# Kernel tuning notes

Hardware: AMD Instinct MI355X
Metric: run time of the kernel (lower is better)

Reference implementation:

```python
import jax, jax.numpy as jnp
import numpy as np

EMB_DIM = 128
MID = 192  # ceil(1.5 * emb_dim)
VOCAB = 3000
KCLS = 5
B = 16
S = 128
EPS = 1e-5


def _linear_init(k, fin, fout):
    k1, k2 = jax.random.split(k)
    bound = 1.0 / np.sqrt(fin)
    W = jax.random.uniform(k1, (fin, fout), minval=-bound, maxval=bound, dtype=jnp.float32)
    b = jax.random.uniform(k2, (fout,), minval=-bound, maxval=bound, dtype=jnp.float32)
    return W, b


def setup_inputs() -> dict:
    key = jax.random.key(0)
    ks = jax.random.split(key, 7)
    emb = jax.random.normal(ks[0], (VOCAB, EMB_DIM), dtype=jnp.float32)
    W1, b1 = _linear_init(ks[1], 2 * EMB_DIM, MID)   # encoder layer 1
    W2, b2 = _linear_init(ks[2], MID, EMB_DIM)       # encoder layer 2
    W3, b3 = _linear_init(ks[3], EMB_DIM, MID)       # decoder layer 1
    W4, b4 = _linear_init(ks[4], MID, 2 * EMB_DIM)   # decoder layer 2
    Wk, bk = _linear_init(ks[5], EMB_DIM, KCLS)      # soft head
    inputs = jax.random.randint(ks[6], (B, S), 0, VOCAB, dtype=jnp.int64)
    return dict(inputs=inputs, emb=emb, W1=W1, b1=b1, W2=W2, b2=b2,
                W3=W3, b3=b3, W4=W4, b4=b4, Wk=Wk, bk=bk)


def _forward(inputs, emb, W1, b1, W2, b2, W3, b3, W4, b4, Wk, bk):
    X = emb[inputs]                      # (B,S,m)
    Bs, Sl, m = X.shape
    bidx = jnp.arange(Bs)
    karr = jnp.arange(Sl)
    jarr = jnp.arange(Sl - 1)

    def step(carry, t):
        nodes, counts, acc = carry       # (B,S,m), (B,S), (B,)
        L = Sl - t                       # current active list length
        right, left = nodes[:, 1:], nodes[:, :-1]          # pair j = (node[j+1], node[j])
        y = (jnp.concatenate([right, left], -1) @ W1 + b1) @ W2 + b2   # (B,S-1,m)
        xx = (y @ W3 + b3) @ W4 + b4                                    # (B,S-1,2m)
        # torch cross_entropy with float-vector target: -sum(target * log_softmax(input))
        ls1 = -(right * jax.nn.log_softmax(xx[..., :m], -1)).sum(-1)
        ls2 = -(left * jax.nn.log_softmax(xx[..., m:], -1)).sum(-1)
        n1, n2 = counts[:, 1:], counts[:, :-1]
        loss = ((n1 + EPS) * ls1 + (n2 + EPS) * ls2) / (n1 + n2 + EPS)
        valid = jarr < (L - 1)                                          # only first L-1 pairs active
        idx = jnp.argmin(jnp.where(valid[None, :], loss, jnp.inf), axis=1)  # (B,)
        acc = acc + jnp.take_along_axis(loss, idx[:, None], 1)[:, 0]
        father_x = jnp.take_along_axis(y, idx[:, None, None], 1)[:, 0]  # (B,m)
        # faithful bug: lc = nodelist[idx-1] (python wrap to L-1 when idx==0), rc = nodelist[idx]
        lc_idx = jnp.where(idx == 0, L - 1, idx - 1)
        father_cnt = (jnp.take_along_axis(counts, idx[:, None], 1)[:, 0]
                      + jnp.take_along_axis(counts, lc_idx[:, None], 1)[:, 0])
        pos = jnp.maximum(idx - 1, 0)
        # new list: drop lc and rc, father lands at pos; gather map reproduces list insert/remove
        src = jnp.where((idx[:, None] == 0) | (karr[None, :] < idx[:, None] - 1),
                        karr[None, :], karr[None, :] + 1)
        src = jnp.minimum(src, Sl - 1)
        nodes = jnp.take_along_axis(nodes, src[:, :, None], 1).at[bidx, pos].set(father_x)
        counts = jnp.take_along_axis(counts, src, 1).at[bidx, pos].set(father_cnt)
        return (nodes, counts, acc), None

    init = (X, jnp.ones((Bs, Sl), X.dtype), jnp.zeros((Bs,), X.dtype))
    (nodes, counts, acc), _ = jax.lax.scan(step, init, jnp.arange(Sl - 1))
    pred = jnp.argmax(nodes[:, 0] @ Wk + bk, axis=-1)   # argmax softmax == argmax logits
    return pred, acc.sum() / Bs


def reference(inputs, emb, W1, b1, W2, b2, W3, b3, W4, b4, Wk, bk):
    return _forward(inputs, emb, W1, b1, W2, b2, W3, b3, W4, b4, Wk, bk)
```

## Files before the change

kernel.cpp:

```cpp
#include <hip/hip_runtime.h>
#include <math.h>

#define EMB 128
#define MID 192
#define SEQ 128
#define BATCH 16
#define NPAIR 127
#define KCLS 5
#define EPSF 1e-5f

#define OFF_WYT   0
#define OFF_BY    32768
#define OFF_WXXT  32896
#define OFF_BXX   65664
#define OFF_NODES 65920
#define OFF_YC    328064
#define OFF_L0    588160

__global__ void k_comp(const float* __restrict__ W1, const float* __restrict__ b1,
                       const float* __restrict__ W2, const float* __restrict__ b2,
                       const float* __restrict__ W3, const float* __restrict__ b3,
                       const float* __restrict__ W4, const float* __restrict__ b4,
                       float* __restrict__ ws) {
    int tid = blockIdx.x * blockDim.x + threadIdx.x;
    if (tid < 32768) {
        int k = tid >> 7, o = tid & 127;
        float a = 0.f;
        for (int j = 0; j < MID; ++j) a += W1[k*MID+j] * W2[j*EMB+o];
        int q = k >> 6, jj = k & 63;
        ws[OFF_WYT + (size_t)(q*128 + o)*64 + jj] = a;
    } else if (tid < 65536) {
        int t = tid - 32768;
        int k = t >> 8, c = t & 255;
        float a = 0.f;
        for (int j = 0; j < MID; ++j) a += W3[k*MID+j] * W4[j*256+c];
        int hh = k >> 6, jj = k & 63;
        ws[OFF_WXXT + (size_t)(hh*256 + c)*64 + jj] = a;
    } else if (tid < 65536 + 128) {
        int o = tid - 65536;
        float a = b2[o];
        for (int j = 0; j < MID; ++j) a += b1[j] * W2[j*EMB+o];
        ws[OFF_BY + o] = a;
    } else if (tid < 65536 + 128 + 256) {
        int o = tid - 65536 - 128;
        float a = b4[o];
        for (int j = 0; j < MID; ++j) a += b3[j] * W4[j*256+o];
        ws[OFF_BXX + o] = a;
    }
}

__global__ void k_nodes(const int* __restrict__ inp, const float* __restrict__ emb,
                        float* __restrict__ ws) {
    int tid = blockIdx.x * blockDim.x + threadIdx.x;
    if (tid >= BATCH*SEQ*EMB) return;
    int d = tid & 127;
    int bs = tid >> 7;
    int tok = inp[bs];
    ws[OFF_NODES + tid] = emb[tok*EMB + d];
}

__global__ void __launch_bounds__(512, 2) k_init(float* __restrict__ ws) {
    __shared__ float s_x[2][2*EMB];
    __shared__ float s_red[4][2][EMB];
    __shared__ float s_redx[2][2][256];
    __shared__ float s_y[2][EMB];
    __shared__ float s_by[EMB];
    __shared__ float s_bxx[2*EMB];
    __shared__ float s_ls[2][2];
    int tid = threadIdx.x;
    int b = blockIdx.x >> 3, g = blockIdx.x & 7;
    float wy[64], wxx[64];
    {
        const float4* gw = (const float4*)(ws + OFF_WYT) + (size_t)tid*16;
        #pragma unroll
        for (int i = 0; i < 16; ++i) { float4 v = gw[i]; wy[4*i]=v.x; wy[4*i+1]=v.y; wy[4*i+2]=v.z; wy[4*i+3]=v.w; }
        const float4* gx = (const float4*)(ws + OFF_WXXT) + (size_t)tid*16;
        #pragma unroll
        for (int i = 0; i < 16; ++i) { float4 v = gx[i]; wxx[4*i]=v.x; wxx[4*i+1]=v.y; wxx[4*i+2]=v.z; wxx[4*i+3]=v.w; }
    }
    if (tid < EMB) s_by[tid] = ws[OFF_BY + tid];
    if (tid < 2*EMB) s_bxx[tid] = ws[OFF_BXX + tid];
    const float* nodes = ws + OFF_NODES + (size_t)b*SEQ*EMB;
    float* yc = ws + OFF_YC + (size_t)b*NPAIR*EMB;
    int q4 = tid >> 7, o = tid & 127;
    int hh = tid >> 8, c = tid & 255;
    int p_s = tid >> 8, kk = tid & 255;
    __syncthreads();
    for (int i = 0; i < 8; ++i) {
        int base = g*16 + i*2;
        {
            int j = base + p_s;
            int jj = j < NPAIR ? j : NPAIR - 1;
            s_x[p_s][kk] = nodes[(jj + (kk < 128 ? 1 : 0))*EMB + (kk & 127)];
        }
        __syncthreads();
        float a0 = 0.f, a1 = 0.f;
        #pragma unroll
        for (int j = 0; j < 64; ++j) {
            float w = wy[j];
            a0 += s_x[0][q4*64 + j] * w;
            a1 += s_x[1][q4*64 + j] * w;
        }
        s_red[q4][0][o] = a0;
        s_red[q4][1][o] = a1;
        __syncthreads();
        if (tid < 256) {
            int p = tid >> 7, oo = tid & 127;
            float yv = s_red[0][p][oo] + s_red[1][p][oo] + s_red[2][p][oo] + s_red[3][p][oo] + s_by[oo];
            s_y[p][oo] = yv;
            int j2 = base + p;
            if (j2 < NPAIR) yc[(size_t)j2*EMB + oo] = yv;
        }
        __syncthreads();
        float c0 = 0.f, c1 = 0.f;
        #pragma unroll
        for (int j = 0; j < 64; ++j) {
            float w = wxx[j];
            c0 += s_y[0][hh*64 + j] * w;
            c1 += s_y[1][hh*64 + j] * w;
        }
        s_redx[hh][0][c] = c0;
        s_redx[hh][1][c] = c1;
        __syncthreads();
        if (tid < 256) {
            int w = tid >> 6, lane = tid & 63;
            int p2 = w >> 1, h2 = w & 1;
            int cA = h2*128 + lane, cB = cA + 64;
            float v0 = s_redx[0][p2][cA] + s_redx[1][p2][cA] + s_bxx[cA];
            float v1 = s_redx[0][p2][cB] + s_redx[1][p2][cB] + s_bxx[cB];
            float m = fmaxf(v0, v1);
            for (int s = 32; s; s >>= 1) m = fmaxf(m, __shfl_xor(m, s, 64));
            float se = expf(v0 - m) + expf(v1 - m);
            for (int s = 32; s; s >>= 1) se += __shfl_xor(se, s, 64);
            float lse = m + logf(se);
            float o0 = s_x[p2][cA], o1 = s_x[p2][cB];
            float term = o0*(v0 - lse) + o1*(v1 - lse);
            for (int s = 32; s; s >>= 1) term += __shfl_xor(term, s, 64);
            if (lane == 0) s_ls[p2][h2] = -term;
        }
        __syncthreads();
        if (tid < 2) {
            int j2 = base + tid;
            if (j2 < NPAIR) {
                float l = ((1.f+EPSF)*s_ls[tid][0] + (1.f+EPSF)*s_ls[tid][1]) / (2.f + EPSF);
                ws[OFF_L0 + b*NPAIR + j2] = l;
            }
        }
        __syncthreads();
    }
}

__global__ void __launch_bounds__(512, 2) k_seq(float* __restrict__ ws,
                      const float* __restrict__ Wk, const float* __restrict__ bkv,
                      float* __restrict__ out) {
    __shared__ float s_nodes[SEQ*EMB];
    __shared__ float s_yc[NPAIR*EMB];
    __shared__ float s_x[2][2*EMB];
    __shared__ float s_red[4][2][EMB];
    __shared__ float s_redx[2][2][256];
    __shared__ float s_y[2][EMB];
    __shared__ float s_by[EMB];
    __shared__ float s_bxx[2*EMB];
    __shared__ float s_ls[2][2];
    __shared__ float s_loss[NPAIR];
    __shared__ float s_cnt[SEQ];
    __shared__ int   s_nslot[SEQ];
    __shared__ int   s_yslot[NPAIR];
    __shared__ int   s_q[2];
    __shared__ float s_wv[2];
    __shared__ int   s_wi[2];
    __shared__ float s_log[KCLS];

    int tid = threadIdx.x;
    int b = blockIdx.x;
    float wy[64], wxx[64];
    {
        const float4* gw = (const float4*)(ws + OFF_WYT) + (size_t)tid*16;
        #pragma unroll
        for (int i = 0; i < 16; ++i) { float4 v = gw[i]; wy[4*i]=v.x; wy[4*i+1]=v.y; wy[4*i+2]=v.z; wy[4*i+3]=v.w; }
        const float4* gx = (const float4*)(ws + OFF_WXXT) + (size_t)tid*16;
        #pragma unroll
        for (int i = 0; i < 16; ++i) { float4 v = gx[i]; wxx[4*i]=v.x; wxx[4*i+1]=v.y; wxx[4*i+2]=v.z; wxx[4*i+3]=v.w; }
    }
    {
        const float4* gn = (const float4*)(ws + OFF_NODES + (size_t)b*SEQ*EMB);
        float4* sn = (float4*)s_nodes;
        for (int i = tid; i < SEQ*EMB/4; i += 512) sn[i] = gn[i];
        const float4* gy = (const float4*)(ws + OFF_YC + (size_t)b*NPAIR*EMB);
        float4* sy = (float4*)s_yc;
        for (int i = tid; i < NPAIR*EMB/4; i += 512) sy[i] = gy[i];
    }
    if (tid < EMB) s_by[tid] = ws[OFF_BY + tid];
    if (tid < 2*EMB) s_bxx[tid] = ws[OFF_BXX + tid];
    if (tid < NPAIR) { s_loss[tid] = ws[OFF_L0 + b*NPAIR + tid]; s_yslot[tid] = tid; }
    if (tid < SEQ)   { s_cnt[tid] = 1.f; s_nslot[tid] = tid; }
    float acc = 0.f;
    int q4 = tid >> 7, o = tid & 127;
    int hh = tid >> 8, c = tid & 255;
    int p_s = tid >> 8, kk = tid & 255;
    __syncthreads();

    #pragma unroll 1
    for (int t = 0; t < NPAIR; ++t) {
        int L = SEQ - t;
        if (t > 0) {
            {
                int q = s_q[p_s];
                s_x[p_s][kk] = s_nodes[s_nslot[q + (kk < 128 ? 1 : 0)]*EMB + (kk & 127)];
            }
            __syncthreads();
            float a0 = 0.f, a1 = 0.f;
            #pragma unroll
            for (int j = 0; j < 64; ++j) {
                float w = wy[j];
                a0 += s_x[0][q4*64 + j] * w;
                a1 += s_x[1][q4*64 + j] * w;
            }
            s_red[q4][0][o] = a0;
            s_red[q4][1][o] = a1;
            __syncthreads();
            if (tid < 256) {
                int p = tid >> 7, oo = tid & 127;
                float yv = s_red[0][p][oo] + s_red[1][p][oo] + s_red[2][p][oo] + s_red[3][p][oo] + s_by[oo];
                s_y[p][oo] = yv;
                s_yc[(size_t)s_yslot[s_q[p]]*EMB + oo] = yv;
            }
            __syncthreads();
            float c0 = 0.f, c1 = 0.f;
            #pragma unroll
            for (int j = 0; j < 64; ++j) {
                float w = wxx[j];
                c0 += s_y[0][hh*64 + j] * w;
                c1 += s_y[1][hh*64 + j] * w;
            }
            s_redx[hh][0][c] = c0;
            s_redx[hh][1][c] = c1;
            __syncthreads();
            if (tid < 256) {
                int w = tid >> 6, lane = tid & 63;
                int p2 = w >> 1, h2 = w & 1;
                int cA = h2*128 + lane, cB = cA + 64;
                float v0 = s_redx[0][p2][cA] + s_redx[1][p2][cA] + s_bxx[cA];
                float v1 = s_redx[0][p2][cB] + s_redx[1][p2][cB] + s_bxx[cB];
                float m = fmaxf(v0, v1);
                for (int s = 32; s; s >>= 1) m = fmaxf(m, __shfl_xor(m, s, 64));
                float se = expf(v0 - m) + expf(v1 - m);
                for (int s = 32; s; s >>= 1) se += __shfl_xor(se, s, 64);
                float lse = m + logf(se);
                float o0 = s_x[p2][cA], o1 = s_x[p2][cB];
                float term = o0*(v0 - lse) + o1*(v1 - lse);
                for (int s = 32; s; s >>= 1) term += __shfl_xor(term, s, 64);
                if (lane == 0) s_ls[p2][h2] = -term;
            }
            __syncthreads();
            if (tid < 2) {
                int qq = s_q[tid];
                float n1 = s_cnt[qq+1], n2 = s_cnt[qq];
                s_loss[qq] = ((n1+EPSF)*s_ls[tid][0] + (n2+EPSF)*s_ls[tid][1]) / (n1+n2+EPSF);
            }
            __syncthreads();
        }
        if (tid < 128) {
            float v = (tid < L-1) ? s_loss[tid] : INFINITY;
            int ii = tid;
            for (int s = 32; s; s >>= 1) {
                float ov = __shfl_xor(v, s, 64);
                int   oi = __shfl_xor(ii, s, 64);
                if (ov < v || (ov == v && oi < ii)) { v = ov; ii = oi; }
            }
            if ((tid & 63) == 0) { s_wv[tid>>6] = v; s_wi[tid>>6] = ii; }
        }
        __syncthreads();
        float bv0 = s_wv[0], bv1 = s_wv[1];
        int idx = (s_wv[1] < s_wv[0]) ? s_wi[1] : s_wi[0];
        if (tid == 0) acc += fminf(bv0, bv1);
        int pos = idx > 0 ? idx - 1 : 0;
        int slotF = s_nslot[pos];
        int ysI   = s_yslot[idx];
        float fcnt = s_cnt[idx] + s_cnt[idx == 0 ? L-1 : idx-1];
        bool doShift = (idx > 0);
        bool shL = doShift && tid >= pos+1 && tid <= L-3;
        bool shC = doShift && tid >= pos+1 && tid <= L-2;
        float nl = 0.f, nc = 0.f; int nn = 0, ny = 0;
        if (shL) { nl = s_loss[tid+1]; ny = s_yslot[tid+1]; }
        if (shC) { nc = s_cnt[tid+1];  nn = s_nslot[tid+1]; }
        float fx = (tid < EMB) ? s_yc[(size_t)ysI*EMB + tid] : 0.f;
        __syncthreads();
        if (tid < EMB) s_nodes[slotF*EMB + tid] = fx;
        if (shL) { s_loss[tid] = nl; s_yslot[tid] = ny; }
        if (shC) { s_cnt[tid]  = nc; s_nslot[tid] = nn; }
        if (tid == 0) {
            s_cnt[pos] = fcnt;
            s_q[0] = (pos >= 1) ? pos - 1 : pos;
            s_q[1] = pos;
        }
        __syncthreads();
    }
    if (tid < KCLS) {
        int slot0 = s_nslot[0];
        float a = bkv[tid];
        for (int k = 0; k < EMB; ++k) a += s_nodes[slot0*EMB + k] * Wk[k*KCLS + tid];
        s_log[tid] = a;
    }
    __syncthreads();
    if (tid == 0) {
        int best = 0;
        for (int cc = 1; cc < KCLS; ++cc) if (s_log[cc] > s_log[best]) best = cc;
        out[b] = (float)best;
        atomicAdd(&out[BATCH], acc * (1.f/16.f));
    }
}

extern "C" void kernel_launch(void* const* d_in, const int* in_sizes, int n_in,
                              void* d_out, int out_size, void* d_ws, size_t ws_size,
                              hipStream_t stream) {
    const int*   inp = (const int*)d_in[0];
    const float* emb = (const float*)d_in[1];
    const float* W1  = (const float*)d_in[2];
    const float* b1  = (const float*)d_in[3];
    const float* W2  = (const float*)d_in[4];
    const float* b2  = (const float*)d_in[5];
    const float* W3  = (const float*)d_in[6];
    const float* b3  = (const float*)d_in[7];
    const float* W4  = (const float*)d_in[8];
    const float* b4  = (const float*)d_in[9];
    const float* Wk  = (const float*)d_in[10];
    const float* bk  = (const float*)d_in[11];
    float* out = (float*)d_out;
    float* ws  = (float*)d_ws;

    hipMemsetAsync(d_out, 0, (size_t)out_size * sizeof(float), stream);

    k_comp<<<(65920 + 255) / 256, 256, 0, stream>>>(W1, b1, W2, b2, W3, b3, W4, b4, ws);
    k_nodes<<<(BATCH*SEQ*EMB + 255) / 256, 256, 0, stream>>>(inp, emb, ws);
    k_init<<<BATCH * 8, 512, 0, stream>>>(ws);
    k_seq<<<BATCH, 512, 0, stream>>>(ws, Wk, bk, out);
}
```

Before: 548.7 us.

## Restructure sequential merge loop to cut barriers and use shuffle reductions

Weight layouts are transposed so that adjacent lanes hold the partial sums of one output, which lets the two matvecs reduce with warp shuffles instead of shared-memory partial buffers and extra barriers. The loss/cross-entropy evaluation for the two recomputed pairs now runs concurrently with the argmin over the remaining pairs. The list update is double-buffered, so it is written without a read/write barrier, and the next step's gather slots are precomputed. Launch bounds drop to one block per CU. The aim is to shorten the serial per-step critical path of the 127-step loop, at the cost of more intricate index bookkeeping and a risk in tie-breaking and edge-case correctness.

```diff
diff --git a/kernel.cpp b/kernel.cpp
--- a/kernel.cpp
+++ b/kernel.cpp
@@ -28,14 +28,14 @@
         float a = 0.f;
         for (int j = 0; j < MID; ++j) a += W1[k*MID+j] * W2[j*EMB+o];
         int q = k >> 6, jj = k & 63;
-        ws[OFF_WYT + (size_t)(q*128 + o)*64 + jj] = a;
+        ws[OFF_WYT + (size_t)(o*4 + q)*64 + jj] = a;
     } else if (tid < 65536) {
         int t = tid - 32768;
         int k = t >> 8, c = t & 255;
         float a = 0.f;
         for (int j = 0; j < MID; ++j) a += W3[k*MID+j] * W4[j*256+c];
         int hh = k >> 6, jj = k & 63;
-        ws[OFF_WXXT + (size_t)(hh*256 + c)*64 + jj] = a;
+        ws[OFF_WXXT + (size_t)(c*2 + hh)*64 + jj] = a;
     } else if (tid < 65536 + 128) {
         int o = tid - 65536;
         float a = b2[o];
@@ -59,7 +59,7 @@
     ws[OFF_NODES + tid] = emb[tok*EMB + d];
 }
 
-__global__ void __launch_bounds__(512, 2) k_init(float* __restrict__ ws) {
+__global__ void __launch_bounds__(512, 1) k_init(float* __restrict__ ws) {
     __shared__ float s_x[2][2*EMB];
     __shared__ float s_red[4][2][EMB];
     __shared__ float s_redx[2][2][256];
@@ -71,10 +71,10 @@
     int b = blockIdx.x >> 3, g = blockIdx.x & 7;
     float wy[64], wxx[64];
     {
-        const float4* gw = (const float4*)(ws + OFF_WYT) + (size_t)tid*16;
+        const float4* gw = (const float4*)(ws + OFF_WYT) + ((size_t)(tid & 127)*4 + (tid >> 7))*16;
         #pragma unroll
         for (int i = 0; i < 16; ++i) { float4 v = gw[i]; wy[4*i]=v.x; wy[4*i+1]=v.y; wy[4*i+2]=v.z; wy[4*i+3]=v.w; }
-        const float4* gx = (const float4*)(ws + OFF_WXXT) + (size_t)tid*16;
+        const float4* gx = (const float4*)(ws + OFF_WXXT) + ((size_t)(tid & 255)*2 + (tid >> 8))*16;
         #pragma unroll
         for (int i = 0; i < 16; ++i) { float4 v = gx[i]; wxx[4*i]=v.x; wxx[4*i+1]=v.y; wxx[4*i+2]=v.z; wxx[4*i+3]=v.w; }
     }
@@ -150,25 +150,25 @@
     }
 }
 
-__global__ void __launch_bounds__(512, 2) k_seq(float* __restrict__ ws,
+#define SX(p, c) s_x[p][(((c) >> 6)*72) + ((c) & 63)]
+
+__global__ void __launch_bounds__(512, 1) k_seq(float* __restrict__ ws,
                       const float* __restrict__ Wk, const float* __restrict__ bkv,
                       float* __restrict__ out) {
     __shared__ float s_nodes[SEQ*EMB];
     __shared__ float s_yc[NPAIR*EMB];
-    __shared__ float s_x[2][2*EMB];
-    __shared__ float s_red[4][2][EMB];
-    __shared__ float s_redx[2][2][256];
+    __shared__ float s_x[2][4*72];
     __shared__ float s_y[2][EMB];
+    __shared__ float s_xx[2][2*EMB];
     __shared__ float s_by[EMB];
     __shared__ float s_bxx[2*EMB];
     __shared__ float s_ls[2][2];
-    __shared__ float s_loss[NPAIR];
-    __shared__ float s_cnt[SEQ];
-    __shared__ int   s_nslot[SEQ];
-    __shared__ int   s_yslot[NPAIR];
-    __shared__ int   s_q[2];
-    __shared__ float s_wv[2];
-    __shared__ int   s_wi[2];
+    __shared__ float s_loss[2][SEQ];
+    __shared__ float s_cnt[2][SEQ];
+    __shared__ int   s_nslot[2][SEQ];
+    __shared__ int   s_yslot[2][SEQ];
+    __shared__ float s_restv[2];
+    __shared__ int   s_resti[2];
     __shared__ float s_log[KCLS];
 
     int tid = threadIdx.x;
@@ -192,115 +192,147 @@
     }
     if (tid < EMB) s_by[tid] = ws[OFF_BY + tid];
     if (tid < 2*EMB) s_bxx[tid] = ws[OFF_BXX + tid];
-    if (tid < NPAIR) { s_loss[tid] = ws[OFF_L0 + b*NPAIR + tid]; s_yslot[tid] = tid; }
-    if (tid < SEQ)   { s_cnt[tid] = 1.f; s_nslot[tid] = tid; }
+    if (tid < NPAIR) { s_loss[0][tid] = ws[OFF_L0 + b*NPAIR + tid]; s_yslot[0][tid] = tid; }
+    if (tid < SEQ)   { s_cnt[0][tid] = 1.f; s_nslot[0][tid] = tid; }
+
     float acc = 0.f;
-    int q4 = tid >> 7, o = tid & 127;
-    int hh = tid >> 8, c = tid & 255;
-    int p_s = tid >> 8, kk = tid & 255;
+    int cur = 0;
+    int q0c = -1, q1c = -1;
+    int slotFr = 0, ysIr = 0, myslot = 0;
+    bool stageYc = false;
+    const int q4 = tid & 3,  oy = tid >> 2;
+    const int hh = tid & 1,  cx = tid >> 1;
+    const int sp = tid >> 8, skk = tid & 255;
     __syncthreads();
 
     #pragma unroll 1
     for (int t = 0; t < NPAIR; ++t) {
-        int L = SEQ - t;
+        const int L = SEQ - t;
         if (t > 0) {
+            if (tid < EMB) s_nodes[slotFr*EMB + tid] = s_yc[(size_t)ysIr*EMB + tid];
             {
-                int q = s_q[p_s];
-                s_x[p_s][kk] = s_nodes[s_nslot[q + (kk < 128 ? 1 : 0)]*EMB + (kk & 127)];
+                float xv = stageYc ? s_yc[(size_t)ysIr*EMB + (skk & 127)]
+                                   : s_nodes[myslot*EMB + (skk & 127)];
+                s_x[sp][((skk >> 6)*72) + (skk & 63)] = xv;
             }
             __syncthreads();
-            float a0 = 0.f, a1 = 0.f;
-            #pragma unroll
-            for (int j = 0; j < 64; ++j) {
-                float w = wy[j];
-                a0 += s_x[0][q4*64 + j] * w;
-                a1 += s_x[1][q4*64 + j] * w;
-            }
-            s_red[q4][0][o] = a0;
-            s_red[q4][1][o] = a1;
+            {
+                float a0 = 0.f, a1 = 0.f;
+                const float* x0 = &s_x[0][q4*72];
+                const float* x1 = &s_x[1][q4*72];
+                #pragma unroll
+                for (int j = 0; j < 64; ++j) { float w = wy[j]; a0 += x0[j]*w; a1 += x1[j]*w; }
+                a0 += __shfl_xor(a0, 1, 64); a1 += __shfl_xor(a1, 1, 64);
+                a0 += __shfl_xor(a0, 2, 64); a1 += __shfl_xor(a1, 2, 64);
+                if (q4 == 0) {
+                    float bb = s_by[oy];
+                    float y0 = a0 + bb, y1 = a1 + bb;
+                    s_y[0][oy] = y0; s_y[1][oy] = y1;
+                    s_yc[(size_t)s_yslot[cur][q0c]*EMB + oy] = y0;
+                    s_yc[(size_t)s_yslot[cur][q1c]*EMB + oy] = y1;
+                }
+            }
             __syncthreads();
-            if (tid < 256) {
-                int p = tid >> 7, oo = tid & 127;
-                float yv = s_red[0][p][oo] + s_red[1][p][oo] + s_red[2][p][oo] + s_red[3][p][oo] + s_by[oo];
-                s_y[p][oo] = yv;
-                s_yc[(size_t)s_yslot[s_q[p]]*EMB + oo] = yv;
+            {
+                float c0 = 0.f, c1 = 0.f;
+                const float* y0p = &s_y[0][hh*64];
+                const float* y1p = &s_y[1][hh*64];
+                #pragma unroll
+                for (int j = 0; j < 64; ++j) { float w = wxx[j]; c0 += y0p[j]*w; c1 += y1p[j]*w; }
+                c0 += __shfl_xor(c0, 1, 64); c1 += __shfl_xor(c1, 1, 64);
+                if (hh == 0) {
+                    float bb = s_bxx[cx];
+                    s_xx[0][cx] = c0 + bb;
+                    s_xx[1][cx] = c1 + bb;
+                }
             }
             __syncthreads();
-            float c0 = 0.f, c1 = 0.f;
-            #pragma unroll
-            for (int j = 0; j < 64; ++j) {
-                float w = wxx[j];
-                c0 += s_y[0][hh*64 + j] * w;
-                c1 += s_y[1][hh*64 + j] * w;
-            }
-            s_redx[hh][0][c] = c0;
-            s_redx[hh][1][c] = c1;
-            __syncthreads();
-            if (tid < 256) {
-                int w = tid >> 6, lane = tid & 63;
-                int p2 = w >> 1, h2 = w & 1;
-                int cA = h2*128 + lane, cB = cA + 64;
-                float v0 = s_redx[0][p2][cA] + s_redx[1][p2][cA] + s_bxx[cA];
-                float v1 = s_redx[0][p2][cB] + s_redx[1][p2][cB] + s_bxx[cB];
-                float m = fmaxf(v0, v1);
-                for (int s = 32; s; s >>= 1) m = fmaxf(m, __shfl_xor(m, s, 64));
-                float se = expf(v0 - m) + expf(v1 - m);
-                for (int s = 32; s; s >>= 1) se += __shfl_xor(se, s, 64);
-                float lse = m + logf(se);
-                float o0 = s_x[p2][cA], o1 = s_x[p2][cB];
-                float term = o0*(v0 - lse) + o1*(v1 - lse);
-                for (int s = 32; s; s >>= 1) term += __shfl_xor(term, s, 64);
-                if (lane == 0) s_ls[p2][h2] = -term;
-            }
-            __syncthreads();
-            if (tid < 2) {
-                int qq = s_q[tid];
-                float n1 = s_cnt[qq+1], n2 = s_cnt[qq];
-                s_loss[qq] = ((n1+EPSF)*s_ls[tid][0] + (n2+EPSF)*s_ls[tid][1]) / (n1+n2+EPSF);
-            }
-            __syncthreads();
-        }
-        if (tid < 128) {
-            float v = (tid < L-1) ? s_loss[tid] : INFINITY;
-            int ii = tid;
+        }
+        if (t > 0 && tid < 128) {
+            int p2 = tid >> 6, h2 = (tid >> 5) & 1, l5 = tid & 31;
+            int base = h2*128 + l5;
+            float v0 = s_xx[p2][base],      v1 = s_xx[p2][base+32];
+            float v2 = s_xx[p2][base+64],   v3 = s_xx[p2][base+96];
+            float o0 = SX(p2, base),        o1 = SX(p2, base+32);
+            float o2 = SX(p2, base+64),     o3 = SX(p2, base+96);
+            float m   = fmaxf(fmaxf(v0, v1), fmaxf(v2, v3));
+            float sov = v0*o0 + v1*o1 + v2*o2 + v3*o3;
+            float so  = (o0 + o1) + (o2 + o3);
+            for (int s = 16; s; s >>= 1) {
+                m    = fmaxf(m, __shfl_xor(m, s, 64));
+                sov += __shfl_xor(sov, s, 64);
+                so  += __shfl_xor(so, s, 64);
+            }
+            float se = expf(v0 - m) + expf(v1 - m) + expf(v2 - m) + expf(v3 - m);
+            for (int s = 16; s; s >>= 1) se += __shfl_xor(se, s, 64);
+            if (l5 == 0) s_ls[p2][h2] = (m + logf(se))*so - sov;
+        } else if (tid >= 128 && tid < 256) {
+            int j = tid - 128;
+            float v = (j <= L-2 && j != q0c && j != q1c) ? s_loss[cur][j] : INFINITY;
+            int ii = j;
             for (int s = 32; s; s >>= 1) {
                 float ov = __shfl_xor(v, s, 64);
                 int   oi = __shfl_xor(ii, s, 64);
                 if (ov < v || (ov == v && oi < ii)) { v = ov; ii = oi; }
             }
-            if ((tid & 63) == 0) { s_wv[tid>>6] = v; s_wi[tid>>6] = ii; }
-        }
-        __syncthreads();
-        float bv0 = s_wv[0], bv1 = s_wv[1];
-        int idx = (s_wv[1] < s_wv[0]) ? s_wi[1] : s_wi[0];
-        if (tid == 0) acc += fminf(bv0, bv1);
-        int pos = idx > 0 ? idx - 1 : 0;
-        int slotF = s_nslot[pos];
-        int ysI   = s_yslot[idx];
-        float fcnt = s_cnt[idx] + s_cnt[idx == 0 ? L-1 : idx-1];
-        bool doShift = (idx > 0);
-        bool shL = doShift && tid >= pos+1 && tid <= L-3;
-        bool shC = doShift && tid >= pos+1 && tid <= L-2;
-        float nl = 0.f, nc = 0.f; int nn = 0, ny = 0;
-        if (shL) { nl = s_loss[tid+1]; ny = s_yslot[tid+1]; }
-        if (shC) { nc = s_cnt[tid+1];  nn = s_nslot[tid+1]; }
-        float fx = (tid < EMB) ? s_yc[(size_t)ysI*EMB + tid] : 0.f;
-        __syncthreads();
-        if (tid < EMB) s_nodes[slotF*EMB + tid] = fx;
-        if (shL) { s_loss[tid] = nl; s_yslot[tid] = ny; }
-        if (shC) { s_cnt[tid]  = nc; s_nslot[tid] = nn; }
-        if (tid == 0) {
-            s_cnt[pos] = fcnt;
-            s_q[0] = (pos >= 1) ? pos - 1 : pos;
-            s_q[1] = pos;
-        }
-        __syncthreads();
-    }
-    if (tid < KCLS) {
-        int slot0 = s_nslot[0];
-        float a = bkv[tid];
-        for (int k = 0; k < EMB; ++k) a += s_nodes[slot0*EMB + k] * Wk[k*KCLS + tid];
-        s_log[tid] = a;
+            if ((tid & 63) == 0) { s_restv[(tid >> 6) - 2] = v; s_resti[(tid >> 6) - 2] = ii; }
+        }
+        __syncthreads();
+        float l0 = INFINITY, l1 = INFINITY;
+        if (t > 0) {
+            float n1a = s_cnt[cur][q0c+1], n2a = s_cnt[cur][q0c];
+            l0 = ((n1a + EPSF)*s_ls[0][0] + (n2a + EPSF)*s_ls[0][1]) / (n1a + n2a + EPSF);
+            float n1b = s_cnt[cur][q1c+1], n2b = s_cnt[cur][q1c];
+            l1 = ((n1b + EPSF)*s_ls[1][0] + (n2b + EPSF)*s_ls[1][1]) / (n1b + n2b + EPSF);
+        }
+        float bv = s_restv[0]; int bi = s_resti[0];
+        {
+            float rv = s_restv[1]; int ri = s_resti[1];
+            if (rv < bv || (rv == bv && ri < bi)) { bv = rv; bi = ri; }
+        }
+        if (t > 0) {
+            if (l1 < bv || (l1 == bv && q1c < bi)) { bv = l1; bi = q1c; }
+            if (l0 < bv || (l0 == bv && q0c < bi)) { bv = l0; bi = q0c; }
+        }
+        if (tid == 0) acc += bv;
+        const int idx = bi;
+        const int pos = idx > 0 ? idx - 1 : 0;
+        const bool dS = idx > 0;
+        const float fcnt = s_cnt[cur][idx] + s_cnt[cur][idx == 0 ? L-1 : idx-1];
+        slotFr = s_nslot[cur][pos];
+        ysIr   = s_yslot[cur][idx];
+        const int nxt = cur ^ 1;
+        if (tid < NPAIR) {
+            int sh = (dS && tid >= pos+1 && tid <= L-3) ? 1 : 0;
+            int sj = tid + sh;
+            float v = (sj == q0c) ? l0 : (sj == q1c) ? l1 : s_loss[cur][sj];
+            s_loss[nxt][tid]  = v;
+            s_yslot[nxt][tid] = s_yslot[cur][sj];
+        }
+        if (tid < SEQ) {
+            int sh = (dS && tid >= pos+1 && tid <= L-2) ? 1 : 0;
+            s_cnt[nxt][tid]   = (tid == pos) ? fcnt : s_cnt[cur][tid + sh];
+            s_nslot[nxt][tid] = s_nslot[cur][tid + sh];
+        }
+        q0c = pos >= 1 ? pos - 1 : 0;
+        q1c = pos;
+        {
+            int qq = (sp ? q1c : q0c) + (skk < 128 ? 1 : 0);
+            stageYc = (qq == q1c);
+            int sh = (dS && qq >= pos+1 && qq <= L-2) ? 1 : 0;
+            myslot = s_nslot[cur][qq + sh];
+        }
+        cur = nxt;
+        __syncthreads();
+    }
+    {
+        int w = tid >> 6, l = tid & 63;
+        if (w < KCLS) {
+            const float* root = s_yc + (size_t)ysIr*EMB;
+            float p = root[2*l]*Wk[(2*l)*KCLS + w] + root[2*l+1]*Wk[(2*l+1)*KCLS + w];
+            for (int s = 32; s; s >>= 1) p += __shfl_xor(p, s, 64);
+            if (l == 0) s_log[w] = p + bkv[w];
+        }
     }
     __syncthreads();
     if (tid == 0) {
```

Result: no change. 539.0 us (-1.8%).
